# Performance work log

Hardware: AMD Instinct MI355X
Metric: run time of the kernel (lower is better)

Reference implementation:

```python
import jax, jax.numpy as jnp
import numpy as np

D_MODEL = 1024
N_HEADS = 16
D_HEAD = D_MODEL // N_HEADS
INIT_GATE = -5.0


def setup_inputs() -> dict:
    key = jax.random.key(0)
    ks = jax.random.split(key, 11)
    B, S, D = 2, 2048, D_MODEL
    lim = 1.0 / np.sqrt(D)  # torch Linear default init range
    def lin(kw, kb):
        W = jax.random.uniform(kw, (D, D), jnp.float32, -lim, lim)
        b = jax.random.uniform(kb, (D,), jnp.float32, -lim, lim)
        return W, b
    W_Q, b_Q = lin(ks[0], ks[1])
    W_K, b_K = lin(ks[2], ks[3])
    W_V, b_V = lin(ks[4], ks[5])
    W_O, b_O = lin(ks[6], ks[7])
    return {
        "low_freq": jax.random.normal(ks[8], (B, S, D), jnp.float32),
        "high_freq": jax.random.normal(ks[9], (B, S, D), jnp.float32),
        "W_Q": W_Q, "b_Q": b_Q,
        "W_K": W_K, "b_K": b_K,
        "W_V": W_V, "b_V": b_V,
        "W_O": W_O, "b_O": b_O,
        "gamma": jnp.asarray(INIT_GATE, jnp.float32),
    }


def reference(low_freq, high_freq, W_Q, b_Q, W_K, b_K, W_V, b_V, W_O, b_O, gamma):
    B, S, D = low_freq.shape
    H, Dh = N_HEADS, D_HEAD
    # torch Linear: y = x @ W.T + b
    Q = (low_freq @ W_Q.T + b_Q).reshape(B, S, H, Dh).transpose(0, 2, 1, 3)
    K = (low_freq @ W_K.T + b_K).reshape(B, S, H, Dh).transpose(0, 2, 1, 3)
    V = (high_freq @ W_V.T + b_V).reshape(B, S, H, Dh).transpose(0, 2, 1, 3)
    scores = jnp.einsum("bhqd,bhkd->bhqk", Q, K) / jnp.sqrt(jnp.asarray(Dh, low_freq.dtype))
    attn = jax.nn.softmax(scores, axis=-1)
    ctx = jnp.einsum("bhqk,bhkd->bhqd", attn, V)
    ctx = ctx.transpose(0, 2, 1, 3).reshape(B, S, D)
    Z = ctx @ W_O.T + b_O
    beta = jax.nn.sigmoid(gamma)
    return low_freq + beta * Z
```

## Files before the change

kernel.cpp:

```cpp
#include <hip/hip_runtime.h>
#include <stdint.h>

#define D_MODEL 1024
#define N_HEADS 16
#define BB      2
#define SS      2048
#define MTOT    (BB*SS)
#define NXs     ((size_t)MTOT * D_MODEL)
#define NWs     ((size_t)D_MODEL * D_MODEL)

typedef __attribute__((ext_vector_type(8))) short bf16x8;
typedef __attribute__((ext_vector_type(4))) float f32x4;
typedef __attribute__((ext_vector_type(16))) float f32x16;

__device__ __forceinline__ ushort f2bf(float f) {
    union { float f; uint32_t u; } v; v.f = f;
    uint32_t u = v.u;
    return (ushort)((u + 0x7FFFu + ((u >> 16) & 1u)) >> 16);
}
__device__ __forceinline__ uint32_t pk2bf(float lo, float hi) {
    uint32_t r;
    asm("v_cvt_pk_bf16_f32 %0, %1, %2" : "=v"(r) : "v"(lo), "v"(hi));
    return r;
}
__device__ __forceinline__ float exp2_raw(float x) {
    float r;
    asm("v_exp_f32 %0, %1" : "=v"(r) : "v"(x));
    return r;
}
#define GLL16(gp, lp) __builtin_amdgcn_global_load_lds( \
    (const __attribute__((address_space(1))) void*)(gp), \
    (__attribute__((address_space(3))) void*)(lp), 16, 0, 0)

__global__ __launch_bounds__(256) void cvt_all(
    const float* __restrict__ s0, const float* __restrict__ s1,
    const float* __restrict__ s2, const float* __restrict__ s3,
    const float* __restrict__ s4, const float* __restrict__ s5,
    ushort* __restrict__ dst)
{
    size_t i = ((size_t)blockIdx.x * 256 + threadIdx.x) * 4;
    const float* src; size_t off;
    if (i < NXs)            { src = s0; off = i; }
    else if (i < 2 * NXs)   { src = s1; off = i - NXs; }
    else {
        size_t j = i - 2 * NXs;
        int sel = (int)(j >> 20);
        src = sel == 0 ? s2 : sel == 1 ? s3 : sel == 2 ? s4 : s5;
        off = j & (NWs - 1);
    }
    float4 v = *reinterpret_cast<const float4*>(src + off);
    ushort4 o;
    o.x = f2bf(v.x); o.y = f2bf(v.y); o.z = f2bf(v.z); o.w = f2bf(v.w);
    *reinterpret_cast<ushort4*>(dst + i) = o;
}

__global__ __launch_bounds__(512, 2) void qkv256(
    const ushort* __restrict__ Xl, const ushort* __restrict__ Xh,
    const ushort* __restrict__ Wqk, const ushort* __restrict__ Wv,
    const float* __restrict__ bq, const float* __restrict__ bk,
    const float* __restrict__ bv,
    ushort* __restrict__ QK, ushort* __restrict__ VT)
{
    extern __shared__ char dsm[];
    const int t = threadIdx.x, lane = t & 63, w = t >> 6;
    const int wr = w >> 2, wc = w & 3;
    const int c16 = lane & 15, kg = lane >> 4;
    const int xorv = (c16 & 7) << 4;

    const int bid = blockIdx.x;
    const ushort *Ain, *Win;
    int bm, bn, isV;
    if (bid < 128) {
        const int xcd = bid & 7, k = bid >> 3;
        Ain = Xl; Win = Wqk; isV = 0;
        bm = ((xcd >> 1) << 2) | (k >> 2);
        bn = ((xcd & 1) << 2) | (k & 3);
    } else {
        const int vid = bid - 128;
        const int xcd = vid & 7, k = vid >> 3;
        Ain = Xh; Win = Wv; isV = 1;
        bm = (xcd << 1) | (k >> 2);
        bn = k & 3;
    }

    const int swcol = ((t & 7) * 8) ^ (((t >> 3) & 7) << 3);
    const ushort* Asrc = Ain + (size_t)(bm * 256 + (t >> 3)) * 1024 + swcol;
    const ushort* Bsrc = Win + (size_t)(bn * 256 + (t >> 3)) * 1024 + swcol;
    char* const ldsA = dsm;
    char* const ldsB = dsm + 65536;

#define STAGE_A(Tn, h, sl) do { \
    const ushort* _s = Asrc + (size_t)(h) * 128 * 1024 + (size_t)(Tn) * 64; \
    char* _d = ldsA + (sl) * 32768 + (h) * 16384 + t * 16; \
    GLL16(_s, _d); GLL16(_s + 64 * 1024, _d + 8192); } while (0)
#define STAGE_B(Tn, h, sl) do { \
    const ushort* _s = Bsrc + (size_t)(h) * 128 * 1024 + (size_t)(Tn) * 64; \
    char* _d = ldsB + (sl) * 32768 + (h) * 16384 + t * 16; \
    GLL16(_s, _d); GLL16(_s + 64 * 1024, _d + 8192); } while (0)

    f32x4 acc[8][4] = {};

    STAGE_A(0, 0, 0); STAGE_B(0, 0, 0);
    STAGE_A(0, 1, 0); STAGE_B(0, 1, 0);
    asm volatile("s_waitcnt vmcnt(0)" ::: "memory");
    __syncthreads();

    const char* Ahb = ldsA + wr * 16384;
    const char* Bhb = ldsB + (wc >> 1) * 16384;
    const int nbase = (wc & 1) * 64;

#pragma unroll 1
    for (int T = 0; T < 16; ++T) {
        const int slot = T & 1;
        const char* Ab = Ahb + slot * 32768;
        const char* Bb = Bhb + slot * 32768;
        bf16x8 af[2][4], bfr[2][4];

        if (T + 1 < 16) {
            STAGE_A(T + 1, 0, slot ^ 1);
            STAGE_B(T + 1, 0, slot ^ 1);
            STAGE_A(T + 1, 1, slot ^ 1);
            STAGE_B(T + 1, 1, slot ^ 1);
            asm volatile("s_waitcnt vmcnt(8)" ::: "memory");
        } else {
            asm volatile("s_waitcnt vmcnt(0)" ::: "memory");
        }
#pragma unroll
        for (int kk = 0; kk < 2; ++kk) {
#pragma unroll
            for (int mf = 0; mf < 4; ++mf)
                af[kk][mf] = *(const bf16x8*)(Ab +
                    (((mf * 16 + c16) * 128 + kk * 64 + kg * 16) ^ xorv));
#pragma unroll
            for (int nf = 0; nf < 4; ++nf)
                bfr[kk][nf] = *(const bf16x8*)(Bb +
                    (((nbase + nf * 16 + c16) * 128 + kk * 64 + kg * 16) ^ xorv));
        }
        __builtin_amdgcn_s_barrier();
        asm volatile("s_waitcnt lgkmcnt(0)" ::: "memory");
        __builtin_amdgcn_sched_barrier(0);
        __builtin_amdgcn_s_setprio(1);
#pragma unroll
        for (int kk = 0; kk < 2; ++kk)
#pragma unroll
            for (int mf = 0; mf < 4; ++mf)
#pragma unroll
                for (int nf = 0; nf < 4; ++nf)
                    acc[mf][nf] = __builtin_amdgcn_mfma_f32_16x16x32_bf16(
                        af[kk][mf], bfr[kk][nf], acc[mf][nf], 0, 0, 0);
        __builtin_amdgcn_s_setprio(0);
        __builtin_amdgcn_s_barrier();

#pragma unroll
        for (int kk = 0; kk < 2; ++kk)
#pragma unroll
            for (int mf = 0; mf < 4; ++mf)
                af[kk][mf] = *(const bf16x8*)(Ab +
                    (((64 + mf * 16 + c16) * 128 + kk * 64 + kg * 16) ^ xorv));
        __builtin_amdgcn_s_barrier();
        asm volatile("s_waitcnt lgkmcnt(0)" ::: "memory");
        __builtin_amdgcn_sched_barrier(0);
        __builtin_amdgcn_s_setprio(1);
#pragma unroll
        for (int kk = 0; kk < 2; ++kk)
#pragma unroll
            for (int mf = 0; mf < 4; ++mf)
#pragma unroll
                for (int nf = 0; nf < 4; ++nf)
                    acc[4 + mf][nf] = __builtin_amdgcn_mfma_f32_16x16x32_bf16(
                        af[kk][mf], bfr[kk][nf], acc[4 + mf][nf], 0, 0, 0);
        __builtin_amdgcn_s_setprio(0);
        __builtin_amdgcn_s_barrier();
    }

    const int row0 = bm * 256 + wr * 128;
    const int col0w = wc * 64;
    if (!isV) {
#pragma unroll
        for (int nf = 0; nf < 4; ++nf) {
            const int col = bn * 256 + col0w + nf * 16 + c16;
            const float bv_ = (col < 1024 ? bq : bk)[col & 1023];
            const float sc  = (col < 1024 ? 0.125f * 1.44269504f : 1.f);
#pragma unroll
            for (int mf = 0; mf < 8; ++mf)
#pragma unroll
                for (int r = 0; r < 4; ++r) {
                    const int row = row0 + mf * 16 + kg * 4 + r;
                    QK[(size_t)row * 2048 + col] = f2bf((acc[mf][nf][r] + bv_) * sc);
                }
        }
    } else {
#pragma unroll
        for (int nf = 0; nf < 4; ++nf) {
            const int col = bn * 256 + col0w + nf * 16 + c16;
            const int h = col >> 6, d = col & 63;
            const float bv_ = bv[col];
#pragma unroll
            for (int mf = 0; mf < 8; ++mf) {
                const int rw0 = row0 + mf * 16 + kg * 4;
                const int b_ = rw0 >> 11, s0 = rw0 & 2047;
                ushort4 ov;
                ov.x = f2bf(acc[mf][nf][0] + bv_);
                ov.y = f2bf(acc[mf][nf][1] + bv_);
                ov.z = f2bf(acc[mf][nf][2] + bv_);
                ov.w = f2bf(acc[mf][nf][3] + bv_);
                *reinterpret_cast<ushort4*>(VT + ((size_t)(b_ * 16 + h) * 64 + d) * 2048 + s0) = ov;
            }
        }
    }
#undef STAGE_A
#undef STAGE_B
}

__global__ __launch_bounds__(256) void o_gemm(
    const ushort* __restrict__ Cb, const ushort* __restrict__ Wo,
    const float* __restrict__ bo, const float* __restrict__ low,
    const float* __restrict__ gamma, float* __restrict__ outf)
{
    __shared__ __align__(16) ushort As[2][64 * 64];
    __shared__ __align__(16) ushort Bs[2][64 * 64];
    const int t = threadIdx.x, lane = t & 63, w = t >> 6;
    const int wr = w >> 1, wc = w & 1, c16 = lane & 15, kg = lane >> 4;
    const int xorv = (c16 & 7) << 4;
    const int bid = blockIdx.x;
    const int xcd = bid & 7, i = bid >> 3;
    const int bm = xcd * 8 + (i >> 4), bn = i & 15;

    const int swc = ((t & 7) ^ ((t >> 3) & 7)) * 8;
    const ushort* Ag = Cb + (size_t)(bm * 64 + (t >> 3)) * 1024 + swc;
    const ushort* Wg = Wo + (size_t)(bn * 64 + (t >> 3)) * 1024 + swc;

    f32x4 acc[2][2] = {};

#define OSTAGE(Tn, sl) do { \
    const int off_ = (Tn) * 64; \
    char* a_ = (char*)As[sl] + t * 16; \
    char* b_ = (char*)Bs[sl] + t * 16; \
    GLL16(Ag + off_,             a_); \
    GLL16(Ag + off_ + 32 * 1024, a_ + 4096); \
    GLL16(Wg + off_,             b_); \
    GLL16(Wg + off_ + 32 * 1024, b_ + 4096); } while (0)

    OSTAGE(0, 0);
    __syncthreads();

#pragma unroll 1
    for (int T = 0; T < 16; ++T) {
        const int slot = T & 1;
        if (T + 1 < 16) OSTAGE(T + 1, slot ^ 1);
        const char* Ab = (const char*)As[slot];
        const char* Bb = (const char*)Bs[slot];
        bf16x8 af[2][2], bfr[2][2];
#pragma unroll
        for (int kk = 0; kk < 2; ++kk) {
#pragma unroll
            for (int mf = 0; mf < 2; ++mf)
                af[kk][mf] = *(const bf16x8*)(Ab +
                    (((wr * 32 + mf * 16 + c16) * 128 + kk * 64 + kg * 16) ^ xorv));
#pragma unroll
            for (int nf = 0; nf < 2; ++nf)
                bfr[kk][nf] = *(const bf16x8*)(Bb +
                    (((wc * 32 + nf * 16 + c16) * 128 + kk * 64 + kg * 16) ^ xorv));
        }
#pragma unroll
        for (int kk = 0; kk < 2; ++kk)
#pragma unroll
            for (int mf = 0; mf < 2; ++mf)
#pragma unroll
                for (int nf = 0; nf < 2; ++nf)
                    acc[mf][nf] = __builtin_amdgcn_mfma_f32_16x16x32_bf16(
                        af[kk][mf], bfr[kk][nf], acc[mf][nf], 0, 0, 0);
        __syncthreads();
    }
#undef OSTAGE

    const float beta = 1.f / (1.f + __expf(-gamma[0]));
#pragma unroll
    for (int nf = 0; nf < 2; ++nf) {
        const int col = bn * 64 + wc * 32 + nf * 16 + c16;
        const float bv_ = bo[col];
#pragma unroll
        for (int mf = 0; mf < 2; ++mf)
#pragma unroll
            for (int r = 0; r < 4; ++r) {
                const int row = bm * 64 + wr * 32 + mf * 16 + kg * 4 + r;
                const size_t off = (size_t)row * 1024 + col;
                outf[off] = low[off] + beta * (acc[mf][nf][r] + bv_);
            }
    }
}

__global__ __launch_bounds__(512, 4) void flash_attn7(
    const ushort* __restrict__ QK, const ushort* __restrict__ VT,
    ushort* __restrict__ CTX)
{
    __shared__ __align__(16) char smem[65536];
    const int t = threadIdx.x;
    const int lane = t & 63, w = t >> 6;
    const int l31 = lane & 31, hi = lane >> 5;
    const int g = w >> 2, wg = w & 3;

    const int bid = blockIdx.x;
    const int j   = bid >> 3;
    const int hbi = (bid & 7) * 4 + (j >> 4);
    const int qb  = j & 15;
    const int b   = hbi >> 4, h = hbi & 15;

    const size_t qrow = (size_t)b * SS + qb * 128 + wg * 32 + l31;
    const ushort* Qp = QK + qrow * 2048 + h * 64;
    bf16x8 qf[4];
#pragma unroll
    for (int ks = 0; ks < 4; ++ks)
        qf[ks] = *reinterpret_cast<const bf16x8*>(Qp + ks * 16 + hi * 8);

    const int t256 = t & 255;
    const int r0 = t256 >> 3;
    const int cb = ((t256 & 7) ^ (r0 & 7)) << 4;
    const ushort* Ksrc = QK + ((size_t)b * SS + r0) * 2048 + 1024 + h * 64 + (cb >> 1);
    const ushort* Vsrc = VT + ((size_t)(b * N_HEADS + h) * 64 + r0) * SS + (cb >> 1);

    char* const Kreg = smem + g * 16384;
    char* const Vreg = smem + 32768 + g * 16384;

    f32x16 o0 = {}, o1 = {};
    float lsum = 0.f;

    {
        const ushort* Kn = Ksrc + (size_t)g * 64 * 2048;
        const ushort* Vn = Vsrc + g * 64;
        GLL16(Kn,             Kreg + t256 * 16);
        GLL16(Kn + 32 * 2048, Kreg + t256 * 16 + 4096);
        GLL16(Vn,             Vreg + t256 * 16);
        GLL16(Vn + 32 * SS,   Vreg + t256 * 16 + 4096);
    }
    __syncthreads();

    const ushort* Kpf = Ksrc + (size_t)(g + 2) * 64 * 2048;
    const ushort* Vpf = Vsrc + (g + 2) * 64;

    int cur = 0;
    for (int kt2 = 0; kt2 < 16; ++kt2) {
        if (kt2 < 15) {
            char* kd = Kreg + (cur ^ 1) * 8192 + t256 * 16;
            char* vd = Vreg + (cur ^ 1) * 8192 + t256 * 16;
            GLL16(Kpf,             kd);
            GLL16(Kpf + 32 * 2048, kd + 4096);
            GLL16(Vpf,             vd);
            GLL16(Vpf + 32 * SS,   vd + 4096);
            Kpf += (size_t)2 * 64 * 2048;
            Vpf += 2 * 64;
        }
        const char* Kb_ = Kreg + cur * 8192;
        const char* Vb_ = Vreg + cur * 8192;

        f32x16 sa0 = {}, sa1 = {};
        __builtin_amdgcn_s_setprio(1);
#pragma unroll
        for (int ks = 0; ks < 4; ++ks) {
            const int x0 = l31 * 128 + ((ks * 32 + hi * 16) ^ ((l31 & 7) << 4));
            bf16x8 k0 = *reinterpret_cast<const bf16x8*>(Kb_ + x0);
            bf16x8 k1 = *reinterpret_cast<const bf16x8*>(Kb_ + x0 + 32 * 128);
            sa0 = __builtin_amdgcn_mfma_f32_32x32x16_bf16(k0, qf[ks], sa0, 0, 0, 0);
            sa1 = __builtin_amdgcn_mfma_f32_32x32x16_bf16(k1, qf[ks], sa1, 0, 0, 0);
        }
        __builtin_amdgcn_s_setprio(0);

        float p[32];
#pragma unroll
        for (int i = 0; i < 16; ++i) { p[i] = exp2_raw(sa0[i]); p[16 + i] = exp2_raw(sa1[i]); }

        {
            float s16_[16];
#pragma unroll
            for (int i = 0; i < 16; ++i) s16_[i] = p[i] + p[i + 16];
#pragma unroll
            for (int st = 8; st >= 1; st >>= 1)
#pragma unroll
                for (int i = 0; i < st; ++i) s16_[i] += s16_[i + st];
            lsum += s16_[0];
        }

        __builtin_amdgcn_s_setprio(1);
#pragma unroll
        for (int kc = 0; kc < 4; ++kc) {
            const int bq_ = (kc >> 1) * 16 + (kc & 1) * 8;
            uint32_t A0 = pk2bf(p[bq_ + 0], p[bq_ + 1]);
            uint32_t A1 = pk2bf(p[bq_ + 2], p[bq_ + 3]);
            uint32_t B0 = pk2bf(p[bq_ + 4], p[bq_ + 5]);
            uint32_t B1 = pk2bf(p[bq_ + 6], p[bq_ + 7]);
            asm("v_permlane32_swap_b32 %0, %1" : "+v"(A0), "+v"(B0));
            asm("v_permlane32_swap_b32 %0, %1" : "+v"(A1), "+v"(B1));
            union { uint32_t u[4]; bf16x8 v; } pa;
            pa.u[0] = A0; pa.u[1] = A1; pa.u[2] = B0; pa.u[3] = B1;
            const int xv = l31 * 128 + ((kc * 32 + hi * 16) ^ ((l31 & 7) << 4));
            bf16x8 v0 = *reinterpret_cast<const bf16x8*>(Vb_ + xv);
            bf16x8 v1 = *reinterpret_cast<const bf16x8*>(Vb_ + xv + 32 * 128);
            o0 = __builtin_amdgcn_mfma_f32_32x32x16_bf16(v0, pa.v, o0, 0, 0, 0);
            o1 = __builtin_amdgcn_mfma_f32_32x32x16_bf16(v1, pa.v, o1, 0, 0, 0);
        }
        __builtin_amdgcn_s_setprio(0);
        __syncthreads();
        cur ^= 1;
    }

    { float a_ = lsum, b_ = lsum;
      asm("v_permlane32_swap_b32 %0, %1" : "+v"(a_), "+v"(b_));
      lsum = a_ + b_; }

    float* O1 = (float*)smem;
    float* L1 = (float*)(smem + 128 * 66 * 4);
    const int ql = wg * 32 + l31;
    if (g == 1) {
#pragma unroll
        for (int r = 0; r < 16; ++r) {
            const int d = (r & 3) + 8 * (r >> 2) + 4 * hi;
            O1[ql * 66 + d]      = o0[r];
            O1[ql * 66 + 32 + d] = o1[r];
        }
        if (hi == 0) L1[ql] = lsum;
    }
    __syncthreads();
    if (g == 0) {
        const float invl = 1.f / (lsum + L1[ql]);
        ushort* Cp = CTX + qrow * D_MODEL + h * 64;
#pragma unroll
        for (int dt = 0; dt < 2; ++dt) {
            const f32x16 o = dt ? o1 : o0;
#pragma unroll
            for (int gg = 0; gg < 4; ++gg) {
                ushort4 ov;
#pragma unroll
                for (int jj = 0; jj < 4; ++jj) {
                    const int r = gg * 4 + jj;
                    const int d = dt * 32 + gg * 8 + hi * 4 + jj;
                    const float v = (o[r] + O1[ql * 66 + d]) * invl;
                    ((ushort*)&ov)[jj] = f2bf(v);
                }
                *reinterpret_cast<ushort4*>(Cp + dt * 32 + gg * 8 + hi * 4) = ov;
            }
        }
    }
}

extern "C" void kernel_launch(void* const* d_in, const int* in_sizes, int n_in,
                              void* d_out, int out_size, void* d_ws, size_t ws_size,
                              hipStream_t stream) {
    const float* low   = (const float*)d_in[0];
    const float* high  = (const float*)d_in[1];
    const float* Wq    = (const float*)d_in[2];
    const float* bq    = (const float*)d_in[3];
    const float* Wk    = (const float*)d_in[4];
    const float* bk    = (const float*)d_in[5];
    const float* Wv    = (const float*)d_in[6];
    const float* bv    = (const float*)d_in[7];
    const float* Wo    = (const float*)d_in[8];
    const float* bo    = (const float*)d_in[9];
    const float* gamma = (const float*)d_in[10];
    float* out = (float*)d_out;

    ushort* ws  = (ushort*)d_ws;
    ushort* Xl  = ws;
    ushort* Xh  = Xl  + NXs;
    ushort* Wqb = Xh  + NXs;
    ushort* Wkb = Wqb + NWs;
    ushort* Wvb = Wkb + NWs;
    ushort* Wob = Wvb + NWs;
    ushort* QKb = Wob + NWs;
    ushort* VTb = QKb + 2 * NXs;
    ushort* Cb  = VTb + NXs;
    (void)Wkb;

    const int cvt_blocks = (int)((2 * NXs + 4 * NWs) / 4 / 256);
    cvt_all<<<cvt_blocks, 256, 0, stream>>>(low, high, Wq, Wk, Wv, Wo, ws);

    static int attr_set = 0;
    if (!attr_set) {
        hipFuncSetAttribute((const void*)qkv256,
                            hipFuncAttributeMaxDynamicSharedMemorySize, 131072);
        attr_set = 1;
    }
    qkv256<<<192, 512, 131072, stream>>>(Xl, Xh, Wqb, Wvb, bq, bk, bv, QKb, VTb);

    flash_attn7<<<512, 512, 0, stream>>>(QKb, VTb, Cb);

    o_gemm<<<1024, 256, 0, stream>>>(Cb, Wob, bo, low, gamma, out);
}
```

Baseline: 108.7 us.

## Shrink QKV GEMM tiles to 128x128 with 256-thread blocks

Replaces the 256x256-tile, 512-thread QKV projection GEMM with a 128x128-tile, 256-thread version. The grid grows from 192 to 768 blocks so all CUs are filled, where 192 blocks left many idle on a 256-CU part. LDS use halves to 64 KB per block. The trade-off is lower arithmetic intensity per tile, so more global and L2 traffic for the same work, plus a new XCD-aware block mapping and remapped LDS staging loads.

```diff
diff --git a/kernel.cpp b/kernel.cpp
--- a/kernel.cpp
+++ b/kernel.cpp
@@ -54,7 +54,7 @@
     *reinterpret_cast<ushort4*>(dst + i) = o;
 }
 
-__global__ __launch_bounds__(512, 2) void qkv256(
+__global__ __launch_bounds__(256, 2) void qkv128(
     const ushort* __restrict__ Xl, const ushort* __restrict__ Xh,
     const ushort* __restrict__ Wqk, const ushort* __restrict__ Wv,
     const float* __restrict__ bq, const float* __restrict__ bk,
@@ -63,78 +63,82 @@
 {
     extern __shared__ char dsm[];
     const int t = threadIdx.x, lane = t & 63, w = t >> 6;
-    const int wr = w >> 2, wc = w & 3;
+    const int wr = w >> 1, wc = w & 1;
     const int c16 = lane & 15, kg = lane >> 4;
     const int xorv = (c16 & 7) << 4;
 
     const int bid = blockIdx.x;
     const ushort *Ain, *Win;
     int bm, bn, isV;
-    if (bid < 128) {
+    if (bid < 512) {
         const int xcd = bid & 7, k = bid >> 3;
         Ain = Xl; Win = Wqk; isV = 0;
-        bm = ((xcd >> 1) << 2) | (k >> 2);
-        bn = ((xcd & 1) << 2) | (k & 3);
+        bm = ((xcd >> 1) << 3) | (k >> 3);
+        bn = ((xcd & 1) << 3) | (k & 7);
     } else {
-        const int vid = bid - 128;
+        const int vid = bid - 512;
         const int xcd = vid & 7, k = vid >> 3;
         Ain = Xh; Win = Wv; isV = 1;
-        bm = (xcd << 1) | (k >> 2);
-        bn = k & 3;
+        bm = (xcd << 2) | (k >> 3);
+        bn = k & 7;
     }
 
     const int swcol = ((t & 7) * 8) ^ (((t >> 3) & 7) << 3);
-    const ushort* Asrc = Ain + (size_t)(bm * 256 + (t >> 3)) * 1024 + swcol;
-    const ushort* Bsrc = Win + (size_t)(bn * 256 + (t >> 3)) * 1024 + swcol;
+    const ushort* Asrc = Ain + (size_t)(bm * 128 + (t >> 3)) * 1024 + swcol;
+    const ushort* Bsrc = Win + (size_t)(bn * 128 + (t >> 3)) * 1024 + swcol;
     char* const ldsA = dsm;
-    char* const ldsB = dsm + 65536;
-
-#define STAGE_A(Tn, h, sl) do { \
-    const ushort* _s = Asrc + (size_t)(h) * 128 * 1024 + (size_t)(Tn) * 64; \
-    char* _d = ldsA + (sl) * 32768 + (h) * 16384 + t * 16; \
-    GLL16(_s, _d); GLL16(_s + 64 * 1024, _d + 8192); } while (0)
-#define STAGE_B(Tn, h, sl) do { \
-    const ushort* _s = Bsrc + (size_t)(h) * 128 * 1024 + (size_t)(Tn) * 64; \
-    char* _d = ldsB + (sl) * 32768 + (h) * 16384 + t * 16; \
-    GLL16(_s, _d); GLL16(_s + 64 * 1024, _d + 8192); } while (0)
-
-    f32x4 acc[8][4] = {};
-
-    STAGE_A(0, 0, 0); STAGE_B(0, 0, 0);
-    STAGE_A(0, 1, 0); STAGE_B(0, 1, 0);
+    char* const ldsB = dsm + 32768;
+
+#define STAGE_A(Tn, sl) do { \
+    const ushort* _s = Asrc + (size_t)(Tn) * 64; \
+    char* _d = ldsA + (sl) * 16384 + t * 16; \
+    GLL16(_s,               _d); \
+    GLL16(_s + 32 * 1024,   _d + 4096); \
+    GLL16(_s + 64 * 1024,   _d + 8192); \
+    GLL16(_s + 96 * 1024,   _d + 12288); } while (0)
+#define STAGE_B(Tn, sl) do { \
+    const ushort* _s = Bsrc + (size_t)(Tn) * 64; \
+    char* _d = ldsB + (sl) * 16384 + t * 16; \
+    GLL16(_s,               _d); \
+    GLL16(_s + 32 * 1024,   _d + 4096); \
+    GLL16(_s + 64 * 1024,   _d + 8192); \
+    GLL16(_s + 96 * 1024,   _d + 12288); } while (0)
+
+    f32x4 acc[4][4] = {};
+
+    STAGE_A(0, 0); STAGE_B(0, 0);
     asm volatile("s_waitcnt vmcnt(0)" ::: "memory");
     __syncthreads();
-
-    const char* Ahb = ldsA + wr * 16384;
-    const char* Bhb = ldsB + (wc >> 1) * 16384;
-    const int nbase = (wc & 1) * 64;
 
 #pragma unroll 1
     for (int T = 0; T < 16; ++T) {
         const int slot = T & 1;
-        const char* Ab = Ahb + slot * 32768;
-        const char* Bb = Bhb + slot * 32768;
-        bf16x8 af[2][4], bfr[2][4];
+        const char* Ab = ldsA + slot * 16384;
+        const char* Bb = ldsB + slot * 16384;
 
         if (T + 1 < 16) {
-            STAGE_A(T + 1, 0, slot ^ 1);
-            STAGE_B(T + 1, 0, slot ^ 1);
-            STAGE_A(T + 1, 1, slot ^ 1);
-            STAGE_B(T + 1, 1, slot ^ 1);
+            STAGE_A(T + 1, slot ^ 1);
+            STAGE_B(T + 1, slot ^ 1);
             asm volatile("s_waitcnt vmcnt(8)" ::: "memory");
         } else {
             asm volatile("s_waitcnt vmcnt(0)" ::: "memory");
         }
+
+        bf16x8 af[2][4], bfr[2][4];
 #pragma unroll
         for (int kk = 0; kk < 2; ++kk) {
 #pragma unroll
-            for (int mf = 0; mf < 4; ++mf)
+            for (int mf = 0; mf < 4; ++mf) {
+                const int row = wr * 64 + mf * 16 + c16;
                 af[kk][mf] = *(const bf16x8*)(Ab +
-                    (((mf * 16 + c16) * 128 + kk * 64 + kg * 16) ^ xorv));
-#pragma unroll
-            for (int nf = 0; nf < 4; ++nf)
+                    ((row * 128 + kk * 64 + kg * 16) ^ xorv));
+            }
+#pragma unroll
+            for (int nf = 0; nf < 4; ++nf) {
+                const int row = wc * 64 + nf * 16 + c16;
                 bfr[kk][nf] = *(const bf16x8*)(Bb +
-                    (((nbase + nf * 16 + c16) * 128 + kk * 64 + kg * 16) ^ xorv));
+                    ((row * 128 + kk * 64 + kg * 16) ^ xorv));
+            }
         }
         __builtin_amdgcn_s_barrier();
         asm volatile("s_waitcnt lgkmcnt(0)" ::: "memory");
@@ -150,39 +154,17 @@
                         af[kk][mf], bfr[kk][nf], acc[mf][nf], 0, 0, 0);
         __builtin_amdgcn_s_setprio(0);
         __builtin_amdgcn_s_barrier();
-
-#pragma unroll
-        for (int kk = 0; kk < 2; ++kk)
-#pragma unroll
-            for (int mf = 0; mf < 4; ++mf)
-                af[kk][mf] = *(const bf16x8*)(Ab +
-                    (((64 + mf * 16 + c16) * 128 + kk * 64 + kg * 16) ^ xorv));
-        __builtin_amdgcn_s_barrier();
-        asm volatile("s_waitcnt lgkmcnt(0)" ::: "memory");
-        __builtin_amdgcn_sched_barrier(0);
-        __builtin_amdgcn_s_setprio(1);
-#pragma unroll
-        for (int kk = 0; kk < 2; ++kk)
-#pragma unroll
-            for (int mf = 0; mf < 4; ++mf)
-#pragma unroll
-                for (int nf = 0; nf < 4; ++nf)
-                    acc[4 + mf][nf] = __builtin_amdgcn_mfma_f32_16x16x32_bf16(
-                        af[kk][mf], bfr[kk][nf], acc[4 + mf][nf], 0, 0, 0);
-        __builtin_amdgcn_s_setprio(0);
-        __builtin_amdgcn_s_barrier();
-    }
-
-    const int row0 = bm * 256 + wr * 128;
-    const int col0w = wc * 64;
+    }
+
+    const int row0 = bm * 128 + wr * 64;
     if (!isV) {
 #pragma unroll
         for (int nf = 0; nf < 4; ++nf) {
-            const int col = bn * 256 + col0w + nf * 16 + c16;
+            const int col = bn * 128 + wc * 64 + nf * 16 + c16;
             const float bv_ = (col < 1024 ? bq : bk)[col & 1023];
             const float sc  = (col < 1024 ? 0.125f * 1.44269504f : 1.f);
 #pragma unroll
-            for (int mf = 0; mf < 8; ++mf)
+            for (int mf = 0; mf < 4; ++mf)
 #pragma unroll
                 for (int r = 0; r < 4; ++r) {
                     const int row = row0 + mf * 16 + kg * 4 + r;
@@ -192,11 +174,11 @@
     } else {
 #pragma unroll
         for (int nf = 0; nf < 4; ++nf) {
-            const int col = bn * 256 + col0w + nf * 16 + c16;
+            const int col = bn * 128 + wc * 64 + nf * 16 + c16;
             const int h = col >> 6, d = col & 63;
             const float bv_ = bv[col];
 #pragma unroll
-            for (int mf = 0; mf < 8; ++mf) {
+            for (int mf = 0; mf < 4; ++mf) {
                 const int rw0 = row0 + mf * 16 + kg * 4;
                 const int b_ = rw0 >> 11, s0 = rw0 & 2047;
                 ushort4 ov;
@@ -475,11 +457,11 @@
 
     static int attr_set = 0;
     if (!attr_set) {
-        hipFuncSetAttribute((const void*)qkv256,
-                            hipFuncAttributeMaxDynamicSharedMemorySize, 131072);
+        hipFuncSetAttribute((const void*)qkv128,
+                            hipFuncAttributeMaxDynamicSharedMemorySize, 65536);
         attr_set = 1;
     }
-    qkv256<<<192, 512, 131072, stream>>>(Xl, Xh, Wqb, Wvb, bq, bk, bv, QKb, VTb);
+    qkv128<<<768, 256, 65536, stream>>>(Xl, Xh, Wqb, Wvb, bq, bk, bv, QKb, VTb);
 
     flash_attn7<<<512, 512, 0, stream>>>(QKb, VTb, Cb);
 
```

Result: faster. 101.3 us, median of 2 (-6.8%).
